# Kernel optimization log

Hardware: AMD Instinct MI355X
Metric: run time of the kernel (lower is better)

Reference implementation:

```python
import jax, jax.numpy as jnp
import numpy as np

N, E, IN_DIM, HID, H, D = 50000, 800000, 1280, 256, 4, 64  # gat_out_dim = H*D = HID
NEG_SLOPE = 0.2


def setup_inputs() -> dict:
    key = jax.random.key(0)
    ks = jax.random.split(key, 20)

    def lin(k, fi, fo):
        return (jax.random.normal(k, (fi, fo), jnp.float32) / np.float32(np.sqrt(fi)))

    inp = {
        "x": jax.random.normal(ks[0], (N, IN_DIM), jnp.float32),
        "edge_index": jax.random.randint(ks[1], (2, E), 0, N, dtype=jnp.int32),
        "enc_W": lin(ks[2], IN_DIM, HID), "enc_b": jnp.zeros((HID,), jnp.float32),
        "Wl0": lin(ks[3], HID, H * D), "bl0": jnp.zeros((H * D,), jnp.float32),
        "Wr0": lin(ks[4], HID, H * D), "br0": jnp.zeros((H * D,), jnp.float32),
        "att0": jax.random.normal(ks[5], (H, D), jnp.float32) / np.float32(np.sqrt(D)),
        "bias0": jnp.zeros((H * D,), jnp.float32),
        "Wl1": lin(ks[6], HID, H * D), "bl1": jnp.zeros((H * D,), jnp.float32),
        "Wr1": lin(ks[7], HID, H * D), "br1": jnp.zeros((H * D,), jnp.float32),
        "att1": jax.random.normal(ks[8], (H, D), jnp.float32) / np.float32(np.sqrt(D)),
        "bias1": jnp.zeros((H * D,), jnp.float32),
        "clf_W": lin(ks[9], HID, 1), "clf_b": jnp.zeros((1,), jnp.float32),
    }
    return inp


def gatv2_layer(x, src, dst, Wl, bl, Wr, br, att, bias):
    # x: [N, HID]; src/dst: [E'] with self-loops already appended
    xl = (x @ Wl + bl).reshape(N, H, D)  # source transform
    xr = (x @ Wr + br).reshape(N, H, D)  # target transform
    e = jax.nn.leaky_relu(xl[src] + xr[dst], NEG_SLOPE)   # [E', H, D]
    logits = jnp.einsum('ehd,hd->eh', e, att)              # [E', H]
    # segment softmax over destination nodes (every node has a self-loop)
    m = jax.ops.segment_max(logits, dst, num_segments=N)   # [N, H]
    a = jnp.exp(logits - m[dst])
    denom = jax.ops.segment_sum(a, dst, num_segments=N)
    alpha = a / (denom[dst] + 1e-16)                       # [E', H]
    out = jax.ops.segment_sum(xl[src] * alpha[:, :, None], dst, num_segments=N)
    out = out.reshape(N, H * D) + bias
    out = out + x  # residual (in_dim == out_features -> identity residual); dropout is eval-mode no-op
    return jax.nn.elu(out), alpha


def reference(x, edge_index, enc_W, enc_b, Wl0, bl0, Wr0, br0, att0, bias0,
              Wl1, bl1, Wr1, br1, att1, bias1, clf_W, clf_b):
    # add self loops (PyG GATv2Conv default)
    loops = jnp.arange(N, dtype=edge_index.dtype)
    src = jnp.concatenate([edge_index[0], loops])
    dst = jnp.concatenate([edge_index[1], loops])

    h = x @ enc_W + enc_b                                  # node encoder [N, HID]
    h, alpha0 = gatv2_layer(h, src, dst, Wl0, bl0, Wr0, br0, att0, bias0)
    h, alpha1 = gatv2_layer(h, src, dst, Wl1, bl1, Wr1, br1, att1, bias1)
    preds = (h @ clf_W + clf_b).squeeze(-1)                # [N]
    return preds, alpha0, alpha1
```

## Files before the change

### kernel.cpp

```cpp
#include <hip/hip_runtime.h>
#include <hip/hip_bf16.h>
#include <math.h>

#define N_NODES 50000
#define E_EDGES 800000
#define EP (E_EDGES + N_NODES)
#define IN_DIM 1280
#define HID 256
#define NHEAD 4
#define DHEAD 64
#define NEG_SLOPE 0.2f

typedef unsigned short ushort_t;
typedef __attribute__((ext_vector_type(8))) short short8;
typedef __attribute__((ext_vector_type(4))) float floatx4;

__device__ __forceinline__ void split_bf16(float x, ushort_t& hi, ushort_t& lo) {
  unsigned u = __float_as_uint(x);
  hi = (ushort_t)(u >> 16);
  float rem = x - __uint_as_float(u & 0xFFFF0000u);
  lo = (ushort_t)(__float_as_uint(rem) >> 16);
}

__device__ __forceinline__ void gload_lds16(const void* g, void* l) {
  __builtin_amdgcn_global_load_lds(
      (const __attribute__((address_space(1))) unsigned int*)g,
      (__attribute__((address_space(3))) unsigned int*)l, 16, 0, 0);
}


__global__ void hist_kernel(const int* __restrict__ ei, int* __restrict__ deg) {
  int e = blockIdx.x * blockDim.x + threadIdx.x;
  if (e >= EP) return;
  int dst = (e < E_EDGES) ? ei[E_EDGES + e] : (e - E_EDGES);
  atomicAdd(&deg[dst], 1);
}

__global__ __launch_bounds__(1024) void scan_kernel(int* __restrict__ dc, int* __restrict__ row_ptr) {
  __shared__ int wsum[16];
  int tid = threadIdx.x;
  int lane = tid & 63;
  int wid = tid >> 6;
  int running = 0;
  if (tid == 0) row_ptr[0] = 0;
  for (int base = 0; base < N_NODES; base += 1024) {
    int i = base + tid;
    int v = (i < N_NODES) ? dc[i] : 0;
    int s = v;
    #pragma unroll
    for (int off = 1; off < 64; off <<= 1) {
      int t = __shfl_up(s, off);
      if (lane >= off) s += t;
    }
    if (lane == 63) wsum[wid] = s;
    __syncthreads();
    if (wid == 0 && lane < 16) {
      int w = wsum[lane];
      #pragma unroll
      for (int off = 1; off < 16; off <<= 1) {
        int t = __shfl_up(w, off);
        if (lane >= off) w += t;
      }
      wsum[lane] = w;
    }
    __syncthreads();
    int woff = (wid > 0) ? wsum[wid - 1] : 0;
    int incl = running + woff + s;
    if (i < N_NODES) {
      row_ptr[i + 1] = incl;
      dc[i] = incl - v;
    }
    running += wsum[15];
    __syncthreads();
  }
}

__global__ void scatter_kernel(const int* __restrict__ ei, int* __restrict__ cursor,
                               int* __restrict__ csr_src, int* __restrict__ csr_eid) {
  int e = blockIdx.x * blockDim.x + threadIdx.x;
  if (e >= EP) return;
  int src, dst;
  if (e < E_EDGES) { src = ei[e]; dst = ei[E_EDGES + e]; }
  else             { src = dst = e - E_EDGES; }
  int pos = atomicAdd(&cursor[dst], 1);
  csr_src[pos] = src;
  csr_eid[pos] = e;
}

__global__ void wsplit_packed(const float* __restrict__ W, ushort_t* __restrict__ Ph,
                              ushort_t* __restrict__ Pl, int K, int Nc, int NcT, int colOff) {
  int idx = blockIdx.x * blockDim.x + threadIdx.x;
  if (idx >= K * Nc) return;
  int k = idx / Nc, n = idx - k * Nc;
  ushort_t hi, lo;
  split_bf16(W[idx], hi, lo);
  size_t pi = ((size_t)(k >> 3) * NcT + colOff + n) * 8 + (k & 7);
  Ph[pi] = hi;
  Pl[pi] = lo;
}

__global__ __launch_bounds__(256, 3) void gemm128(const float* __restrict__ A,
                                                  const ushort_t* __restrict__ Bh,
                                                  const ushort_t* __restrict__ Bl,
                                                  const float* __restrict__ bias_l,
                                                  const float* __restrict__ bias_r,
                                                  float* __restrict__ C_l,
                                                  float* __restrict__ C_r,
                                                  int M, int K, int NcT, int Nsplit) {
  __shared__ ushort_t sAh[128 * 40];
  __shared__ ushort_t sAl[128 * 40];
  __shared__ ushort_t sBh[128 * 32];
  __shared__ ushort_t sBl[128 * 32];

  const int tid = threadIdx.x;
  const int lane = tid & 63;
  const int w = tid >> 6;
  const int wm = w >> 1, wn = w & 1;
  const int bm = blockIdx.x * 128;
  const int bn = blockIdx.y * 128;
  const int r = lane & 15, q = lane >> 4;

  floatx4 acc[4][4];
  #pragma unroll
  for (int i = 0; i < 4; ++i)
    #pragma unroll
    for (int j = 0; j < 4; ++j) acc[i][j] = (floatx4)(0.0f);

  const int arow = tid >> 1, achunk = tid & 1;
  int ag = bm + arow; if (ag >= M) ag = M - 1;
  const float* aptr = A + (size_t)ag * K + achunk * 16;
  const int awoff = arow * 40 + achunk * 16;

  const int e0 = tid, e1 = tid + 256;
  const size_t b0base = ((size_t)(e0 >> 7) * NcT + bn + (e0 & 127)) * 8;
  const size_t b1base = ((size_t)(e1 >> 7) * NcT + bn + (e1 & 127)) * 8;

  for (int k0 = 0; k0 < K; k0 += 32) {
    size_t kadd = (size_t)(k0 >> 3) * NcT * 8;
    gload_lds16(Bh + b0base + kadd, &sBh[e0 * 8]);
    gload_lds16(Bh + b1base + kadd, &sBh[e1 * 8]);
    gload_lds16(Bl + b0base + kadd, &sBl[e0 * 8]);
    gload_lds16(Bl + b1base + kadd, &sBl[e1 * 8]);

    #pragma unroll
    for (int hh = 0; hh < 2; ++hh) {
      float va[8];
      *(float4*)&va[0] = *(const float4*)(aptr + k0 + hh * 8);
      *(float4*)&va[4] = *(const float4*)(aptr + k0 + hh * 8 + 4);
      short8 hv, lv;
      #pragma unroll
      for (int i = 0; i < 8; ++i) {
        ushort_t hi, lo;
        split_bf16(va[i], hi, lo);
        hv[i] = (short)hi; lv[i] = (short)lo;
      }
      *(short8*)&sAh[awoff + hh * 8] = hv;
      *(short8*)&sAl[awoff + hh * 8] = lv;
    }

    __syncthreads();

    short8 ah[4], al[4];
    #pragma unroll
    for (int i = 0; i < 4; ++i) {
      int off = (wm * 64 + i * 16 + r) * 40 + q * 8;
      ah[i] = *(const short8*)&sAh[off];
      al[i] = *(const short8*)&sAl[off];
    }
    #pragma unroll
    for (int j = 0; j < 4; ++j) {
      int off = (q * 128 + wn * 64 + j * 16 + r) * 8;
      short8 bh = *(const short8*)&sBh[off];
      short8 bl = *(const short8*)&sBl[off];
      #pragma unroll
      for (int i = 0; i < 4; ++i) {
        acc[i][j] = __builtin_amdgcn_mfma_f32_16x16x32_bf16(ah[i], bh, acc[i][j], 0, 0, 0);
        acc[i][j] = __builtin_amdgcn_mfma_f32_16x16x32_bf16(ah[i], bl, acc[i][j], 0, 0, 0);
        acc[i][j] = __builtin_amdgcn_mfma_f32_16x16x32_bf16(al[i], bh, acc[i][j], 0, 0, 0);
      }
    }
    __syncthreads();
  }

  #pragma unroll
  for (int j = 0; j < 4; ++j) {
    int cg = bn + wn * 64 + j * 16 + r;
    bool sec = cg >= Nsplit;
    int cc = sec ? cg - Nsplit : cg;
    float bv = sec ? bias_r[cc] : bias_l[cc];
    float* Cb = sec ? C_r : C_l;
    #pragma unroll
    for (int i = 0; i < 4; ++i) {
      int row0 = bm + wm * 64 + i * 16 + q * 4;
      #pragma unroll
      for (int rr = 0; rr < 4; ++rr) {
        int row = row0 + rr;
        if (row < M) Cb[(size_t)row * HID + cc] = acc[i][j][rr] + bv;
      }
    }
  }
}

__global__ __launch_bounds__(64) void gat_layer(const float* __restrict__ xl,
                                                const float* __restrict__ xr,
                                                float* h_inout,
                                                const float* __restrict__ att,
                                                const float* __restrict__ bias,
                                                const int* __restrict__ row_ptr,
                                                const int* __restrict__ csr_src,
                                                const int* __restrict__ csr_eid,
                                                float* __restrict__ logits_ws,
                                                float* __restrict__ alpha_out) {
  int node = blockIdx.x;
  int l = threadIdx.x;
  int hgrp = l >> 4;
  int r0 = row_ptr[node];
  int r1 = row_ptr[node + 1];

  float4 xr4 = *(const float4*)(xr + (size_t)node * HID + l * 4);
  float4 at4 = *(const float4*)(att + l * 4);

  float m = -INFINITY;
  float den = 0.f;
  float4 acc = make_float4(0.f, 0.f, 0.f, 0.f);
  for (int j = r0; j < r1; ++j) {
    int s = csr_src[j];
    float4 v = *(const float4*)(xl + (size_t)s * HID + l * 4);
    float t0 = v.x + xr4.x; t0 = (t0 > 0.f) ? t0 : NEG_SLOPE * t0;
    float t1 = v.y + xr4.y; t1 = (t1 > 0.f) ? t1 : NEG_SLOPE * t1;
    float t2 = v.z + xr4.z; t2 = (t2 > 0.f) ? t2 : NEG_SLOPE * t2;
    float t3 = v.w + xr4.w; t3 = (t3 > 0.f) ? t3 : NEG_SLOPE * t3;
    float p = t0 * at4.x + t1 * at4.y + t2 * at4.z + t3 * at4.w;
    p += __shfl_xor(p, 1);
    p += __shfl_xor(p, 2);
    p += __shfl_xor(p, 4);
    p += __shfl_xor(p, 8);
    if ((l & 15) == 0) logits_ws[(size_t)j * NHEAD + hgrp] = p;
    float m_new = fmaxf(m, p);
    float scale = __expf(m - m_new);
    float wgt = __expf(p - m_new);
    den = den * scale + wgt;
    acc.x = acc.x * scale + wgt * v.x;
    acc.y = acc.y * scale + wgt * v.y;
    acc.z = acc.z * scale + wgt * v.z;
    acc.w = acc.w * scale + wgt * v.w;
    m = m_new;
  }
  float inv_den = 1.f / (den + 1e-16f);

  float4 b4 = *(const float4*)(bias + l * 4);
  float4 h4 = *(const float4*)(h_inout + (size_t)node * HID + l * 4);
  float o0 = acc.x * inv_den + b4.x + h4.x;
  float o1 = acc.y * inv_den + b4.y + h4.y;
  float o2 = acc.z * inv_den + b4.z + h4.z;
  float o3 = acc.w * inv_den + b4.w + h4.w;
  o0 = (o0 > 0.f) ? o0 : (__expf(o0) - 1.f);
  o1 = (o1 > 0.f) ? o1 : (__expf(o1) - 1.f);
  o2 = (o2 > 0.f) ? o2 : (__expf(o2) - 1.f);
  o3 = (o3 > 0.f) ? o3 : (__expf(o3) - 1.f);
  *(float4*)(h_inout + (size_t)node * HID + l * 4) = make_float4(o0, o1, o2, o3);

  __threadfence_block();

  float mh = __shfl(m, (l & 3) * 16);
  float dh = __shfl(den, (l & 3) * 16);
  float invd = 1.f / (dh + 1e-16f);
  for (int j = r0 + (l >> 2); j < r1; j += 16) {
    float lg = logits_ws[(size_t)j * NHEAD + (l & 3)];
    alpha_out[(size_t)csr_eid[j] * NHEAD + (l & 3)] = __expf(lg - mh) * invd;
  }
}

__global__ __launch_bounds__(64) void clf_kernel(const float* __restrict__ h,
                                                 const float* __restrict__ clf_W,
                                                 const float* __restrict__ clf_b,
                                                 float* __restrict__ preds) {
  int n = blockIdx.x;
  int l = threadIdx.x;
  float4 v = *(const float4*)(h + (size_t)n * HID + l * 4);
  float4 w = *(const float4*)(clf_W + l * 4);
  float s = v.x * w.x + v.y * w.y + v.z * w.z + v.w * w.w;
  s += __shfl_xor(s, 1);
  s += __shfl_xor(s, 2);
  s += __shfl_xor(s, 4);
  s += __shfl_xor(s, 8);
  s += __shfl_xor(s, 16);
  s += __shfl_xor(s, 32);
  if (l == 0) preds[n] = s + clf_b[0];
}

static inline char* carve(char*& p, size_t bytes) {
  char* ret = p;
  p += (bytes + 255) & ~(size_t)255;
  return ret;
}

extern "C" void kernel_launch(void* const* d_in, const int* in_sizes, int n_in,
                              void* d_out, int out_size, void* d_ws, size_t ws_size,
                              hipStream_t stream) {
  const float* x     = (const float*)d_in[0];
  const int*   ei    = (const int*)d_in[1];
  const float* enc_W = (const float*)d_in[2];
  const float* enc_b = (const float*)d_in[3];
  const float* Wl0   = (const float*)d_in[4];
  const float* bl0   = (const float*)d_in[5];
  const float* Wr0   = (const float*)d_in[6];
  const float* br0   = (const float*)d_in[7];
  const float* att0  = (const float*)d_in[8];
  const float* bias0 = (const float*)d_in[9];
  const float* Wl1   = (const float*)d_in[10];
  const float* bl1   = (const float*)d_in[11];
  const float* Wr1   = (const float*)d_in[12];
  const float* br1   = (const float*)d_in[13];
  const float* att1  = (const float*)d_in[14];
  const float* bias1 = (const float*)d_in[15];
  const float* clf_W = (const float*)d_in[16];
  const float* clf_b = (const float*)d_in[17];

  float* preds  = (float*)d_out;
  float* alpha0 = preds + N_NODES;
  float* alpha1 = alpha0 + (size_t)EP * NHEAD;

  char* p = (char*)d_ws;
  float* h      = (float*)carve(p, (size_t)N_NODES * HID * 4);
  float* xl     = (float*)carve(p, (size_t)N_NODES * HID * 4);
  float* xr     = (float*)carve(p, (size_t)N_NODES * HID * 4);
  float* logits = (float*)carve(p, (size_t)EP * NHEAD * 4);
  int* row_ptr  = (int*)carve(p, (size_t)(N_NODES + 1) * 4);
  int* cursor   = (int*)carve(p, (size_t)N_NODES * 4);
  int* csr_src  = (int*)carve(p, (size_t)EP * 4);
  int* csr_eid  = (int*)carve(p, (size_t)EP * 4);
  ushort_t* encPh = (ushort_t*)carve(p, (size_t)IN_DIM * HID * 2);
  ushort_t* encPl = (ushort_t*)carve(p, (size_t)IN_DIM * HID * 2);
  ushort_t* P0h   = (ushort_t*)carve(p, (size_t)HID * 512 * 2);
  ushort_t* P0l   = (ushort_t*)carve(p, (size_t)HID * 512 * 2);
  ushort_t* P1h   = (ushort_t*)carve(p, (size_t)HID * 512 * 2);
  ushort_t* P1l   = (ushort_t*)carve(p, (size_t)HID * 512 * 2);

  hipMemsetAsync(cursor, 0, N_NODES * sizeof(int), stream);
  int eb = 256, eg = (EP + eb - 1) / eb;
  hist_kernel<<<eg, eb, 0, stream>>>(ei, cursor);
  scan_kernel<<<1, 1024, 0, stream>>>(cursor, row_ptr);
  scatter_kernel<<<eg, eb, 0, stream>>>(ei, cursor, csr_src, csr_eid);

  int wt = 256;
  wsplit_packed<<<(IN_DIM * HID + wt - 1) / wt, wt, 0, stream>>>(enc_W, encPh, encPl, IN_DIM, HID, HID, 0);
  wsplit_packed<<<(HID * HID + wt - 1) / wt, wt, 0, stream>>>(Wl0, P0h, P0l, HID, HID, 512, 0);
  wsplit_packed<<<(HID * HID + wt - 1) / wt, wt, 0, stream>>>(Wr0, P0h, P0l, HID, HID, 512, 256);
  wsplit_packed<<<(HID * HID + wt - 1) / wt, wt, 0, stream>>>(Wl1, P1h, P1l, HID, HID, 512, 0);
  wsplit_packed<<<(HID * HID + wt - 1) / wt, wt, 0, stream>>>(Wr1, P1h, P1l, HID, HID, 512, 256);

  const int MB = (N_NODES + 127) / 128;
  dim3 bGemm(256);

  gemm128<<<dim3(MB, 2), bGemm, 0, stream>>>(x, encPh, encPl, enc_b, enc_b, h, h,
                                             N_NODES, IN_DIM, HID, HID);

  gemm128<<<dim3(MB, 4), bGemm, 0, stream>>>(h, P0h, P0l, bl0, br0, xl, xr,
                                             N_NODES, HID, 512, HID);
  gat_layer<<<N_NODES, 64, 0, stream>>>(xl, xr, h, att0, bias0, row_ptr, csr_src, csr_eid, logits, alpha0);

  gemm128<<<dim3(MB, 4), bGemm, 0, stream>>>(h, P1h, P1l, bl1, br1, xl, xr,
                                             N_NODES, HID, 512, HID);
  gat_layer<<<N_NODES, 64, 0, stream>>>(xl, xr, h, att1, bias1, row_ptr, csr_src, csr_eid, logits, alpha1);

  clf_kernel<<<N_NODES, 64, 0, stream>>>(h, clf_W, clf_b, preds);
}
```

Baseline: 1.089 ms.

## Double-buffer LDS tiles in split-bf16 GEMM to overlap loads with MFMA

Adds ping-pong shared-memory buffers for the A and B tiles of the split-bf16 GEMM. The next K-tile's global loads and async LDS copies are issued before the current tile's MFMAs, and the A split/store happens after them. This needs one barrier per iteration instead of two and hides global-load latency. LDS use doubles, so launch bounds drop from 3 to 2 blocks per CU, which reduces occupancy.

```diff
diff --git a/kernel.cpp b/kernel.cpp
--- a/kernel.cpp
+++ b/kernel.cpp
@@ -99,7 +99,23 @@
   Pl[pi] = lo;
 }
 
-__global__ __launch_bounds__(256, 3) void gemm128(const float* __restrict__ A,
+__device__ __forceinline__ void split_store16(const float* va, ushort_t* dAh,
+                                              ushort_t* dAl, int awoff) {
+  #pragma unroll
+  for (int hh = 0; hh < 2; ++hh) {
+    short8 hv, lv;
+    #pragma unroll
+    for (int i = 0; i < 8; ++i) {
+      ushort_t hi, lo;
+      split_bf16(va[hh * 8 + i], hi, lo);
+      hv[i] = (short)hi; lv[i] = (short)lo;
+    }
+    *(short8*)&dAh[awoff + hh * 8] = hv;
+    *(short8*)&dAl[awoff + hh * 8] = lv;
+  }
+}
+
+__global__ __launch_bounds__(256, 2) void gemm128(const float* __restrict__ A,
                                                   const ushort_t* __restrict__ Bh,
                                                   const ushort_t* __restrict__ Bl,
                                                   const float* __restrict__ bias_l,
@@ -107,10 +123,10 @@
                                                   float* __restrict__ C_l,
                                                   float* __restrict__ C_r,
                                                   int M, int K, int NcT, int Nsplit) {
-  __shared__ ushort_t sAh[128 * 40];
-  __shared__ ushort_t sAl[128 * 40];
-  __shared__ ushort_t sBh[128 * 32];
-  __shared__ ushort_t sBl[128 * 32];
+  __shared__ ushort_t sAh[2][128 * 40];
+  __shared__ ushort_t sAl[2][128 * 40];
+  __shared__ ushort_t sBh[2][128 * 32];
+  __shared__ ushort_t sBl[2][128 * 32];
 
   const int tid = threadIdx.x;
   const int lane = tid & 63;
@@ -135,43 +151,51 @@
   const size_t b0base = ((size_t)(e0 >> 7) * NcT + bn + (e0 & 127)) * 8;
   const size_t b1base = ((size_t)(e1 >> 7) * NcT + bn + (e1 & 127)) * 8;
 
-  for (int k0 = 0; k0 < K; k0 += 32) {
-    size_t kadd = (size_t)(k0 >> 3) * NcT * 8;
-    gload_lds16(Bh + b0base + kadd, &sBh[e0 * 8]);
-    gload_lds16(Bh + b1base + kadd, &sBh[e1 * 8]);
-    gload_lds16(Bl + b0base + kadd, &sBl[e0 * 8]);
-    gload_lds16(Bl + b1base + kadd, &sBl[e1 * 8]);
-
-    #pragma unroll
-    for (int hh = 0; hh < 2; ++hh) {
-      float va[8];
-      *(float4*)&va[0] = *(const float4*)(aptr + k0 + hh * 8);
-      *(float4*)&va[4] = *(const float4*)(aptr + k0 + hh * 8 + 4);
-      short8 hv, lv;
-      #pragma unroll
-      for (int i = 0; i < 8; ++i) {
-        ushort_t hi, lo;
-        split_bf16(va[i], hi, lo);
-        hv[i] = (short)hi; lv[i] = (short)lo;
-      }
-      *(short8*)&sAh[awoff + hh * 8] = hv;
-      *(short8*)&sAl[awoff + hh * 8] = lv;
-    }
-
-    __syncthreads();
+  const int nt = K >> 5;
+
+  {
+    gload_lds16(Bh + b0base, &sBh[0][e0 * 8]);
+    gload_lds16(Bh + b1base, &sBh[0][e1 * 8]);
+    gload_lds16(Bl + b0base, &sBl[0][e0 * 8]);
+    gload_lds16(Bl + b1base, &sBl[0][e1 * 8]);
+    float va[16];
+    *(float4*)&va[0]  = *(const float4*)(aptr + 0);
+    *(float4*)&va[4]  = *(const float4*)(aptr + 4);
+    *(float4*)&va[8]  = *(const float4*)(aptr + 8);
+    *(float4*)&va[12] = *(const float4*)(aptr + 12);
+    split_store16(va, sAh[0], sAl[0], awoff);
+  }
+  __syncthreads();
+
+  int cur = 0;
+  for (int t = 0; t < nt; ++t) {
+    const bool has_next = (t + 1 < nt);
+    float va[16];
+    if (has_next) {
+      const int k0n = (t + 1) << 5;
+      *(float4*)&va[0]  = *(const float4*)(aptr + k0n + 0);
+      *(float4*)&va[4]  = *(const float4*)(aptr + k0n + 4);
+      *(float4*)&va[8]  = *(const float4*)(aptr + k0n + 8);
+      *(float4*)&va[12] = *(const float4*)(aptr + k0n + 12);
+      size_t kadd = (size_t)(k0n >> 3) * NcT * 8;
+      gload_lds16(Bh + b0base + kadd, &sBh[cur ^ 1][e0 * 8]);
+      gload_lds16(Bh + b1base + kadd, &sBh[cur ^ 1][e1 * 8]);
+      gload_lds16(Bl + b0base + kadd, &sBl[cur ^ 1][e0 * 8]);
+      gload_lds16(Bl + b1base + kadd, &sBl[cur ^ 1][e1 * 8]);
+    }
 
     short8 ah[4], al[4];
     #pragma unroll
     for (int i = 0; i < 4; ++i) {
       int off = (wm * 64 + i * 16 + r) * 40 + q * 8;
-      ah[i] = *(const short8*)&sAh[off];
-      al[i] = *(const short8*)&sAl[off];
+      ah[i] = *(const short8*)&sAh[cur][off];
+      al[i] = *(const short8*)&sAl[cur][off];
     }
     #pragma unroll
     for (int j = 0; j < 4; ++j) {
       int off = (q * 128 + wn * 64 + j * 16 + r) * 8;
-      short8 bh = *(const short8*)&sBh[off];
-      short8 bl = *(const short8*)&sBl[off];
+      short8 bh = *(const short8*)&sBh[cur][off];
+      short8 bl = *(const short8*)&sBl[cur][off];
       #pragma unroll
       for (int i = 0; i < 4; ++i) {
         acc[i][j] = __builtin_amdgcn_mfma_f32_16x16x32_bf16(ah[i], bh, acc[i][j], 0, 0, 0);
@@ -179,7 +203,11 @@
         acc[i][j] = __builtin_amdgcn_mfma_f32_16x16x32_bf16(al[i], bh, acc[i][j], 0, 0, 0);
       }
     }
+
+    if (has_next) split_store16(va, sAh[cur ^ 1], sAl[cur ^ 1], awoff);
+
     __syncthreads();
+    cur ^= 1;
   }
 
   #pragma unroll
```

Result: no change. 1.098 ms (+0.8%).

## Double-buffer GEMM B tiles and load A directly into MFMA registers

Applied to the files above, without the earlier changes.

The GEMM now loads A fragments straight from global memory into registers in MFMA layout and splits them into bf16 hi/lo there, so the A tiles no longer pass through LDS. The B tiles are double-buffered in LDS, with loads for the next k-tile issued before computing the current one. Hand-placed vmcnt/lgkmcnt waits and raw s_barrier calls replace the __syncthreads pairs to overlap memory with MFMA work. The cost is many more registers (two 32-float A buffers), so launch bounds drop from 3 to 2 blocks per CU. A rows are also reloaded by each wn-wave pair, and the loop assumes an even tile count with fragile waitcnt accounting.

```diff
diff --git a/kernel.cpp b/kernel.cpp
--- a/kernel.cpp
+++ b/kernel.cpp
@@ -99,7 +99,7 @@
   Pl[pi] = lo;
 }
 
-__global__ __launch_bounds__(256, 3) void gemm128(const float* __restrict__ A,
+__global__ __launch_bounds__(256, 2) void gemm128(const float* __restrict__ A,
                                                   const ushort_t* __restrict__ Bh,
                                                   const ushort_t* __restrict__ Bl,
                                                   const float* __restrict__ bias_l,
@@ -107,10 +107,8 @@
                                                   float* __restrict__ C_l,
                                                   float* __restrict__ C_r,
                                                   int M, int K, int NcT, int Nsplit) {
-  __shared__ ushort_t sAh[128 * 40];
-  __shared__ ushort_t sAl[128 * 40];
-  __shared__ ushort_t sBh[128 * 32];
-  __shared__ ushort_t sBl[128 * 32];
+  __shared__ ushort_t sBh[2][128 * 32];
+  __shared__ ushort_t sBl[2][128 * 32];
 
   const int tid = threadIdx.x;
   const int lane = tid & 63;
@@ -126,60 +124,103 @@
     #pragma unroll
     for (int j = 0; j < 4; ++j) acc[i][j] = (floatx4)(0.0f);
 
-  const int arow = tid >> 1, achunk = tid & 1;
-  int ag = bm + arow; if (ag >= M) ag = M - 1;
-  const float* aptr = A + (size_t)ag * K + achunk * 16;
-  const int awoff = arow * 40 + achunk * 16;
+  const float* aAddr0;
+  const float* aAddr1;
+  const float* aAddr2;
+  const float* aAddr3;
+  {
+    int r0 = bm + wm * 64 + r;
+    int r1 = r0 + 16, r2 = r0 + 32, r3 = r0 + 48;
+    if (r0 >= M) r0 = M - 1;
+    if (r1 >= M) r1 = M - 1;
+    if (r2 >= M) r2 = M - 1;
+    if (r3 >= M) r3 = M - 1;
+    aAddr0 = A + (size_t)r0 * K + q * 8;
+    aAddr1 = A + (size_t)r1 * K + q * 8;
+    aAddr2 = A + (size_t)r2 * K + q * 8;
+    aAddr3 = A + (size_t)r3 * K + q * 8;
+  }
 
   const int e0 = tid, e1 = tid + 256;
   const size_t b0base = ((size_t)(e0 >> 7) * NcT + bn + (e0 & 127)) * 8;
   const size_t b1base = ((size_t)(e1 >> 7) * NcT + bn + (e1 & 127)) * 8;
 
-  for (int k0 = 0; k0 < K; k0 += 32) {
+  const int nt = K >> 5;
+
+  float vaA[32], vaB[32];
+  short8 ah[4], al[4];
+
+  auto issueA = [&](float* va, int k0) {
+    *(float4*)&va[0]  = *(const float4*)(aAddr0 + k0);
+    *(float4*)&va[4]  = *(const float4*)(aAddr0 + k0 + 4);
+    *(float4*)&va[8]  = *(const float4*)(aAddr1 + k0);
+    *(float4*)&va[12] = *(const float4*)(aAddr1 + k0 + 4);
+    *(float4*)&va[16] = *(const float4*)(aAddr2 + k0);
+    *(float4*)&va[20] = *(const float4*)(aAddr2 + k0 + 4);
+    *(float4*)&va[24] = *(const float4*)(aAddr3 + k0);
+    *(float4*)&va[28] = *(const float4*)(aAddr3 + k0 + 4);
+  };
+  auto issueB = [&](int buf, int k0) {
     size_t kadd = (size_t)(k0 >> 3) * NcT * 8;
-    gload_lds16(Bh + b0base + kadd, &sBh[e0 * 8]);
-    gload_lds16(Bh + b1base + kadd, &sBh[e1 * 8]);
-    gload_lds16(Bl + b0base + kadd, &sBl[e0 * 8]);
-    gload_lds16(Bl + b1base + kadd, &sBl[e1 * 8]);
-
-    #pragma unroll
-    for (int hh = 0; hh < 2; ++hh) {
-      float va[8];
-      *(float4*)&va[0] = *(const float4*)(aptr + k0 + hh * 8);
-      *(float4*)&va[4] = *(const float4*)(aptr + k0 + hh * 8 + 4);
+    gload_lds16(Bh + b0base + kadd, &sBh[buf][e0 * 8]);
+    gload_lds16(Bh + b1base + kadd, &sBh[buf][e1 * 8]);
+    gload_lds16(Bl + b0base + kadd, &sBl[buf][e0 * 8]);
+    gload_lds16(Bl + b1base + kadd, &sBl[buf][e1 * 8]);
+  };
+  auto splitA = [&](const float* va) {
+    #pragma unroll
+    for (int i = 0; i < 4; ++i) {
       short8 hv, lv;
       #pragma unroll
-      for (int i = 0; i < 8; ++i) {
+      for (int u = 0; u < 8; ++u) {
         ushort_t hi, lo;
-        split_bf16(va[i], hi, lo);
-        hv[i] = (short)hi; lv[i] = (short)lo;
+        split_bf16(va[i * 8 + u], hi, lo);
+        hv[u] = (short)hi; lv[u] = (short)lo;
       }
-      *(short8*)&sAh[awoff + hh * 8] = hv;
-      *(short8*)&sAl[awoff + hh * 8] = lv;
-    }
-
-    __syncthreads();
-
-    short8 ah[4], al[4];
-    #pragma unroll
-    for (int i = 0; i < 4; ++i) {
-      int off = (wm * 64 + i * 16 + r) * 40 + q * 8;
-      ah[i] = *(const short8*)&sAh[off];
-      al[i] = *(const short8*)&sAl[off];
-    }
+      ah[i] = hv; al[i] = lv;
+    }
+  };
+  auto computeTile = [&](int buf) {
+    short8 bh[4], bl[4];
     #pragma unroll
     for (int j = 0; j < 4; ++j) {
       int off = (q * 128 + wn * 64 + j * 16 + r) * 8;
-      short8 bh = *(const short8*)&sBh[off];
-      short8 bl = *(const short8*)&sBl[off];
+      bh[j] = *(const short8*)&sBh[buf][off];
+      bl[j] = *(const short8*)&sBl[buf][off];
+    }
+    asm volatile("s_waitcnt lgkmcnt(0)" ::: "memory");
+    __builtin_amdgcn_s_barrier();
+    #pragma unroll
+    for (int j = 0; j < 4; ++j)
       #pragma unroll
       for (int i = 0; i < 4; ++i) {
-        acc[i][j] = __builtin_amdgcn_mfma_f32_16x16x32_bf16(ah[i], bh, acc[i][j], 0, 0, 0);
-        acc[i][j] = __builtin_amdgcn_mfma_f32_16x16x32_bf16(ah[i], bl, acc[i][j], 0, 0, 0);
-        acc[i][j] = __builtin_amdgcn_mfma_f32_16x16x32_bf16(al[i], bh, acc[i][j], 0, 0, 0);
+        acc[i][j] = __builtin_amdgcn_mfma_f32_16x16x32_bf16(ah[i], bh[j], acc[i][j], 0, 0, 0);
+        acc[i][j] = __builtin_amdgcn_mfma_f32_16x16x32_bf16(ah[i], bl[j], acc[i][j], 0, 0, 0);
+        acc[i][j] = __builtin_amdgcn_mfma_f32_16x16x32_bf16(al[i], bh[j], acc[i][j], 0, 0, 0);
       }
-    }
-    __syncthreads();
+  };
+
+  issueA(vaA, 0);
+  issueB(0, 0);
+
+  for (int t = 0; t < nt; t += 2) {
+    issueA(vaB, (t + 1) << 5);
+    issueB(1, (t + 1) << 5);
+    asm volatile("s_waitcnt vmcnt(12)" ::: "memory");
+    splitA(vaA);
+    __builtin_amdgcn_s_barrier();
+    computeTile(0);
+
+    if (t + 2 < nt) {
+      issueA(vaA, (t + 2) << 5);
+      issueB(0, (t + 2) << 5);
+      asm volatile("s_waitcnt vmcnt(12)" ::: "memory");
+    } else {
+      asm volatile("s_waitcnt vmcnt(0)" ::: "memory");
+    }
+    splitA(vaB);
+    __builtin_amdgcn_s_barrier();
+    computeTile(1);
   }
 
   #pragma unroll
```

Measured after the change: 1.223 ms. 12.3% more time.
